# Kernel tuning notes

Measured on AMD Instinct MI355X. Metric: run time of the kernel, lower is better.

## Reference

```python
import jax, jax.numpy as jnp
import numpy as np

N_HEADS = 16

def setup_inputs() -> dict:
    key = jax.random.key(0)
    k1, k2 = jax.random.split(key)
    B, N, D = 2, 2048, 1024
    hidden_states = jax.random.normal(k1, (B, N, D), dtype=jnp.float32)
    # init std = initializer_range / sqrt(2 * num_layers * hidden_size)
    std = 0.02 / np.sqrt(2.0 * 24 * D)
    queries_weight = jax.random.normal(k2, (D, D), dtype=jnp.float32) * std
    return {"hidden_states": hidden_states, "queries_weight": queries_weight}

def reference(hidden_states, queries_weight):
    # DenseAttention, causal quadratic variant, multi-head, no relpe.
    B, N, D = hidden_states.shape
    H = N_HEADS
    hd = D // H
    # Q = X @ Wq, split into heads -> [B, H, N, hd]
    q = (hidden_states @ queries_weight).reshape(B, N, H, hd).transpose(0, 2, 1, 3)
    # K provided transposed per head -> [B, H, hd, N]; V -> [B, H, N, hd]
    xh = hidden_states.reshape(B, N, H, hd)
    k = xh.transpose(0, 2, 3, 1)
    v = xh.transpose(0, 2, 1, 3)
    # pre_attn = tril(Q @ K)  (no softmax in DenseAttention)
    pre_attn = jnp.tril(jnp.einsum('bhnd,bhdm->bhnm', q, k))  # [B,H,N,N]
    attn = jnp.einsum('bhnm,bhmd->bhnd', pre_attn, v)          # [B,H,N,hd]
    return attn.transpose(0, 2, 1, 3).reshape(B, N, D)
```

## Files before the change

kernel.cpp:

```cpp
#include <hip/hip_runtime.h>
#include <stdint.h>

#define Bz 2
#define Nseq 2048
#define Dm 1024
#define Hh 16
#define NCHUNK 32
#define BK 64

typedef _Float16 half_t;
typedef __attribute__((ext_vector_type(8))) _Float16 h8v;
typedef __attribute__((ext_vector_type(4))) _Float16 h4v;
typedef __attribute__((ext_vector_type(4))) float f4v;

#define GLDS(g, l)                                                        \
  __builtin_amdgcn_global_load_lds(                                       \
      (const __attribute__((address_space(1))) void*)(g),                 \
      (__attribute__((address_space(3))) void*)(l), 16, 0, 0)

__global__ __launch_bounds__(256) void prep_fused(const float* __restrict__ X,
                                                  const float* __restrict__ W,
                                                  half_t* __restrict__ Xf,
                                                  float* __restrict__ U,
                                                  half_t* __restrict__ WT) {
  __shared__ double smem_[2304];
  int bx = blockIdx.x;
  int t = threadIdx.x;
  if (bx < 1024) {
    half_t(*xt)[72] = (half_t(*)[72])smem_;
    half_t(*xtT)[72] = (half_t(*)[72])(smem_ + 1152);
    int c = bx & 31, h = (bx >> 5) & 15, b = bx >> 9;
    int r = t >> 2, c16 = (t & 3) * 16;
    {
      const float* src = X + ((size_t)b * Nseq + c * 64 + r) * Dm + h * 64 + c16;
      half_t* dXf = Xf + ((size_t)b * Nseq + c * 64 + r) * Dm + h * 64 + c16;
      h8v v0, v1;
#pragma unroll
      for (int j = 0; j < 8; j++) { v0[j] = (half_t)src[j]; v1[j] = (half_t)src[8 + j]; }
      *(h8v*)&xt[r][c16] = v0;
      *(h8v*)&xt[r][c16 + 8] = v1;
      *(h8v*)&dXf[0] = v0;
      *(h8v*)&dXf[8] = v1;
    }
    __syncthreads();
    {
      int d = r, mg = c16;
      h8v v0, v1;
#pragma unroll
      for (int j = 0; j < 8; j++) { v0[j] = xt[mg + j][d]; v1[j] = xt[mg + 8 + j][d]; }
      *(h8v*)&xtT[d][mg] = v0;
      *(h8v*)&xtT[d][mg + 8] = v1;
    }
    __syncthreads();
    int wave = t >> 6, lane = t & 63;
    int lrow = lane & 15, lk = (lane >> 4) * 8;
    h8v a0 = *(h8v*)&xtT[wave * 16 + lrow][lk];
    h8v a1 = *(h8v*)&xtT[wave * 16 + lrow][32 + lk];
    f4v acc[4] = {};
#pragma unroll
    for (int j = 0; j < 4; j++) {
      acc[j] = __builtin_amdgcn_mfma_f32_16x16x32_f16(a0, *(h8v*)&xtT[j * 16 + lrow][lk], acc[j], 0, 0, 0);
      acc[j] = __builtin_amdgcn_mfma_f32_16x16x32_f16(a1, *(h8v*)&xtT[j * 16 + lrow][32 + lk], acc[j], 0, 0, 0);
    }
    float* ub = U + (size_t)bx * 4096;
#pragma unroll
    for (int j = 0; j < 4; j++)
#pragma unroll
      for (int v = 0; v < 4; v++)
        ub[(size_t)(wave * 16 + (lane >> 4) * 4 + v) * 64 + j * 16 + (lane & 15)] = acc[j][v];
  } else {
    float(*tile)[65] = (float(*)[65])smem_;
    int bw = bx - 1024;
    int tk = bw >> 4, tn = bw & 15;
    int r = t >> 2, c0 = (t & 3) * 16;
    const float* src = W + (size_t)(tk * 64 + r) * Dm + tn * 64 + c0;
#pragma unroll
    for (int j = 0; j < 16; j++) tile[r][c0 + j] = src[j];
    __syncthreads();
    half_t* dst = WT + (size_t)(tn * 64 + r) * Dm + tk * 64 + c0;
    h8v v0, v1;
#pragma unroll
    for (int j = 0; j < 8; j++) {
      v0[j] = (half_t)(tile[c0 + j][r] * 4096.0f);
      v1[j] = (half_t)(tile[c0 + 8 + j][r] * 4096.0f);
    }
    *(h8v*)&dst[0] = v0;
    *(h8v*)&dst[8] = v1;
  }
}

__global__ __launch_bounds__(256) void qgemm16(const half_t* __restrict__ A,
                                               const half_t* __restrict__ Bw,
                                               half_t* __restrict__ Qs) {
  __shared__ half_t sA[128 * BK];
  __shared__ half_t sB[128 * BK];
  int bm = blockIdx.x >> 3, bn = blockIdx.x & 7;
  int t = threadIdx.x;
  int wave = t >> 6, lane = t & 63;
  int wr = wave >> 1, wc = wave & 1;
  int lrow = lane & 15, g4 = lane >> 4;

  int srow = wave * 32 + (lane >> 3);
  int scol = ((lane & 7) ^ (lane >> 3)) * 8;
  const half_t* pA = A + (size_t)(bm * 128 + srow) * Dm + scol;
  const half_t* pB = Bw + (size_t)(bn * 128 + srow) * Dm + scol;
  half_t* ldsA = sA + (size_t)(wave * 32) * BK;
  half_t* ldsB = sB + (size_t)(wave * 32) * BK;

  f4v acc[4][4] = {};
  for (int k0 = 0; k0 < Dm; k0 += BK) {
#pragma unroll
    for (int q = 0; q < 4; q++) {
      GLDS(pA + (size_t)q * 8 * Dm + k0, ldsA + q * 8 * BK);
      GLDS(pB + (size_t)q * 8 * Dm + k0, ldsB + q * 8 * BK);
    }
    __syncthreads();
#pragma unroll
    for (int ks = 0; ks < 2; ks++) {
      h8v af[4], bf[4];
#pragma unroll
      for (int i = 0; i < 4; i++) {
        int rowA = wr * 64 + i * 16 + lrow;
        uint offA = (uint)rowA * 128 + (((uint)(ks * 64 + g4 * 16)) ^ (uint)((rowA & 7) << 4));
        af[i] = *(const h8v*)((const char*)sA + offA);
        int rowB = wc * 64 + i * 16 + lrow;
        uint offB = (uint)rowB * 128 + (((uint)(ks * 64 + g4 * 16)) ^ (uint)((rowB & 7) << 4));
        bf[i] = *(const h8v*)((const char*)sB + offB);
      }
#pragma unroll
      for (int i = 0; i < 4; i++)
#pragma unroll
        for (int j = 0; j < 4; j++)
          acc[i][j] = __builtin_amdgcn_mfma_f32_16x16x32_f16(af[i], bf[j], acc[i][j], 0, 0, 0);
    }
    __syncthreads();
  }
#pragma unroll
  for (int i = 0; i < 4; i++)
#pragma unroll
    for (int j = 0; j < 4; j++) {
      int row = bm * 128 + wr * 64 + i * 16 + (lane >> 4) * 4;
      int col = bn * 128 + wc * 64 + j * 16 + (lane & 15);
#pragma unroll
      for (int v = 0; v < 4; v++)
        Qs[(size_t)(row + v) * Dm + col] = (half_t)(acc[i][j][v] * 0.0625f);
    }
}

__global__ __launch_bounds__(256) void prefix16(const float* __restrict__ U,
                                                half_t* __restrict__ S16) {
  int g = blockIdx.x * 256 + threadIdx.x;
  int bh = g >> 10, e4 = g & 1023;
  const float4* u = (const float4*)(U + (size_t)bh * NCHUNK * 4096) + e4;
  half_t* s = S16 + (size_t)bh * NCHUNK * 4096 + e4 * 4;
  float4 run = {0.f, 0.f, 0.f, 0.f};
  for (int c = 0; c < NCHUNK; c++) {
    h4v sv;
    sv[0] = (half_t)run.x; sv[1] = (half_t)run.y;
    sv[2] = (half_t)run.z; sv[3] = (half_t)run.w;
    *(h4v*)(s + (size_t)c * 4096) = sv;
    float4 uv = u[(size_t)c * 1024];
    run.x += uv.x; run.y += uv.y; run.z += uv.z; run.w += uv.w;
  }
}

__global__ __launch_bounds__(256) void attn16(const half_t* __restrict__ Xf,
                                              const half_t* __restrict__ Qs,
                                              const half_t* __restrict__ S16,
                                              float* __restrict__ out) {
  __shared__ half_t qs[64][72];
  __shared__ half_t ks[64][72];
  __shared__ half_t vts[64][72];
  __shared__ half_t ss[64][72];
  __shared__ half_t pt[64][72];
  int bx = blockIdx.x;
  int c = bx & 31, h = (bx >> 5) & 15, b = bx >> 9;
  int t = threadIdx.x;
  int r = t >> 2, c16 = (t & 3) * 16;
  {
    size_t rowoff = ((size_t)b * Nseq + c * 64 + r) * Dm + h * 64 + c16;
    *(h8v*)&qs[r][c16]     = *(const h8v*)(Qs + rowoff);
    *(h8v*)&qs[r][c16 + 8] = *(const h8v*)(Qs + rowoff + 8);
    *(h8v*)&ks[r][c16]     = *(const h8v*)(Xf + rowoff);
    *(h8v*)&ks[r][c16 + 8] = *(const h8v*)(Xf + rowoff + 8);
    size_t soff = ((size_t)(b * Hh + h) * NCHUNK + c) * 4096 + r * 64 + c16;
    *(h8v*)&ss[r][c16]     = *(const h8v*)(S16 + soff);
    *(h8v*)&ss[r][c16 + 8] = *(const h8v*)(S16 + soff + 8);
  }
  __syncthreads();
  int wave = t >> 6, lane = t & 63;
  int lrow = lane & 15, lk = (lane >> 4) * 8;
  h8v aq0 = *(h8v*)&qs[wave * 16 + lrow][lk];
  h8v aq1 = *(h8v*)&qs[wave * 16 + lrow][32 + lk];
  f4v p[4] = {};
#pragma unroll
  for (int j = 0; j < 4; j++) {
    p[j] = __builtin_amdgcn_mfma_f32_16x16x32_f16(aq0, *(h8v*)&ks[j * 16 + lrow][lk], p[j], 0, 0, 0);
    p[j] = __builtin_amdgcn_mfma_f32_16x16x32_f16(aq1, *(h8v*)&ks[j * 16 + lrow][32 + lk], p[j], 0, 0, 0);
  }
  {
    int d = r, mg = c16;
    h8v v0, v1;
#pragma unroll
    for (int j = 0; j < 8; j++) { v0[j] = ks[mg + j][d]; v1[j] = ks[mg + 8 + j][d]; }
    *(h8v*)&vts[d][mg] = v0;
    *(h8v*)&vts[d][mg + 8] = v1;
  }
  int orow = wave * 16 + (lane >> 4) * 4;
#pragma unroll
  for (int j = 0; j < 4; j++)
#pragma unroll
    for (int v = 0; v < 4; v++) {
      int rr = orow + v, mm = j * 16 + (lane & 15);
      pt[rr][mm] = (half_t)((mm <= rr) ? p[j][v] : 0.f);
    }
  __syncthreads();
  h8v ap0 = *(h8v*)&pt[wave * 16 + lrow][lk];
  h8v ap1 = *(h8v*)&pt[wave * 16 + lrow][32 + lk];
  f4v o[4] = {};
#pragma unroll
  for (int j = 0; j < 4; j++) {
    o[j] = __builtin_amdgcn_mfma_f32_16x16x32_f16(ap0, *(h8v*)&vts[j * 16 + lrow][lk], o[j], 0, 0, 0);
    o[j] = __builtin_amdgcn_mfma_f32_16x16x32_f16(ap1, *(h8v*)&vts[j * 16 + lrow][32 + lk], o[j], 0, 0, 0);
    o[j] = __builtin_amdgcn_mfma_f32_16x16x32_f16(aq0, *(h8v*)&ss[j * 16 + lrow][lk], o[j], 0, 0, 0);
    o[j] = __builtin_amdgcn_mfma_f32_16x16x32_f16(aq1, *(h8v*)&ss[j * 16 + lrow][32 + lk], o[j], 0, 0, 0);
  }
  float* dst = out + ((size_t)b * Nseq + c * 64) * Dm + h * 64;
#pragma unroll
  for (int j = 0; j < 4; j++)
#pragma unroll
    for (int v = 0; v < 4; v++)
      dst[(size_t)(orow + v) * Dm + j * 16 + (lane & 15)] = o[j][v] * 0.00390625f;
}

extern "C" void kernel_launch(void* const* d_in, const int* in_sizes, int n_in,
                              void* d_out, int out_size, void* d_ws, size_t ws_size,
                              hipStream_t stream) {
  const float* X = (const float*)d_in[0];
  const float* W = (const float*)d_in[1];
  float* out = (float*)d_out;

  float* U = (float*)d_ws;
  half_t* Xf = (half_t*)(U + 4194304);
  half_t* Qs = Xf + 4194304;
  half_t* S16 = Qs + 4194304;
  half_t* WT = S16 + 4194304;

  prep_fused<<<1280, 256, 0, stream>>>(X, W, Xf, U, WT);
  qgemm16<<<256, 256, 0, stream>>>(Xf, WT, Qs);
  prefix16<<<128, 256, 0, stream>>>(U, S16);
  attn16<<<1024, 256, 0, stream>>>(Xf, Qs, S16, out);
}
```

Measured before the change: 108.1 us.

## Fuse Q projection GEMM into attention kernel and store chunk sums in fp16

Merges the Q GEMM and the chunked attention into one kernel. Each block computes a 128x64 Q tile, which covers two sequence chunks of one head, using double-buffered LDS loads, then runs the causal intra-chunk attention on it directly from LDS. This removes the Qs global round trip and one launch. The per-chunk KᵀV partial sums are also stored in fp16 instead of fp32, halving that traffic at some precision risk. The trade-offs are a smaller GEMM tile (128x64 instead of 128x128) and a larger LDS footprint per block.

```diff
diff --git a/kernel.cpp b/kernel.cpp
--- a/kernel.cpp
+++ b/kernel.cpp
@@ -6,7 +6,7 @@
 #define Dm 1024
 #define Hh 16
 #define NCHUNK 32
-#define BK 64
+#define BKq 64
 
 typedef _Float16 half_t;
 typedef __attribute__((ext_vector_type(8))) _Float16 h8v;
@@ -21,7 +21,7 @@
 __global__ __launch_bounds__(256) void prep_fused(const float* __restrict__ X,
                                                   const float* __restrict__ W,
                                                   half_t* __restrict__ Xf,
-                                                  float* __restrict__ U,
+                                                  half_t* __restrict__ U16,
                                                   half_t* __restrict__ WT) {
   __shared__ double smem_[2304];
   int bx = blockIdx.x;
@@ -62,12 +62,12 @@
       acc[j] = __builtin_amdgcn_mfma_f32_16x16x32_f16(a0, *(h8v*)&xtT[j * 16 + lrow][lk], acc[j], 0, 0, 0);
       acc[j] = __builtin_amdgcn_mfma_f32_16x16x32_f16(a1, *(h8v*)&xtT[j * 16 + lrow][32 + lk], acc[j], 0, 0, 0);
     }
-    float* ub = U + (size_t)bx * 4096;
+    half_t* ub = U16 + (size_t)bx * 4096;
 #pragma unroll
     for (int j = 0; j < 4; j++)
 #pragma unroll
       for (int v = 0; v < 4; v++)
-        ub[(size_t)(wave * 16 + (lane >> 4) * 4 + v) * 64 + j * 16 + (lane & 15)] = acc[j][v];
+        ub[(size_t)(wave * 16 + (lane >> 4) * 4 + v) * 64 + j * 16 + (lane & 15)] = (half_t)acc[j][v];
   } else {
     float(*tile)[65] = (float(*)[65])smem_;
     int bw = bx - 1024;
@@ -89,148 +89,165 @@
   }
 }
 
-__global__ __launch_bounds__(256) void qgemm16(const half_t* __restrict__ A,
-                                               const half_t* __restrict__ Bw,
-                                               half_t* __restrict__ Qs) {
-  __shared__ half_t sA[128 * BK];
-  __shared__ half_t sB[128 * BK];
-  int bm = blockIdx.x >> 3, bn = blockIdx.x & 7;
+__global__ __launch_bounds__(256) void prefix16(const half_t* __restrict__ U16,
+                                                half_t* __restrict__ S16) {
+  int g = blockIdx.x * 256 + threadIdx.x;
+  int bh = g >> 10, e4 = g & 1023;
+  const half_t* u = U16 + (size_t)bh * NCHUNK * 4096 + e4 * 4;
+  half_t* s = S16 + (size_t)bh * NCHUNK * 4096 + e4 * 4;
+  float r0 = 0, r1 = 0, r2 = 0, r3 = 0;
+  for (int c = 0; c < NCHUNK; c++) {
+    h4v sv;
+    sv[0] = (half_t)r0; sv[1] = (half_t)r1; sv[2] = (half_t)r2; sv[3] = (half_t)r3;
+    *(h4v*)(s + (size_t)c * 4096) = sv;
+    h4v uv = *(const h4v*)(u + (size_t)c * 4096);
+    r0 += (float)uv[0]; r1 += (float)uv[1]; r2 += (float)uv[2]; r3 += (float)uv[3];
+  }
+}
+
+__global__ __launch_bounds__(256) void qgemm_attn(const half_t* __restrict__ Xf,
+                                                  const half_t* __restrict__ WT,
+                                                  const half_t* __restrict__ S16,
+                                                  float* __restrict__ out) {
+  __shared__ __attribute__((aligned(16))) char smem[55296];
+  int bid = blockIdx.x;
+  int logical = (bid & 7) * 64 + (bid >> 3);
+  int bm = logical >> 4;
+  int bn = logical & 15;
   int t = threadIdx.x;
   int wave = t >> 6, lane = t & 63;
   int wr = wave >> 1, wc = wave & 1;
   int lrow = lane & 15, g4 = lane >> 4;
 
-  int srow = wave * 32 + (lane >> 3);
+  int srowA = wave * 32 + (lane >> 3);
+  int srowB = wave * 16 + (lane >> 3);
   int scol = ((lane & 7) ^ (lane >> 3)) * 8;
-  const half_t* pA = A + (size_t)(bm * 128 + srow) * Dm + scol;
-  const half_t* pB = Bw + (size_t)(bn * 128 + srow) * Dm + scol;
-  half_t* ldsA = sA + (size_t)(wave * 32) * BK;
-  half_t* ldsB = sB + (size_t)(wave * 32) * BK;
-
-  f4v acc[4][4] = {};
-  for (int k0 = 0; k0 < Dm; k0 += BK) {
-#pragma unroll
-    for (int q = 0; q < 4; q++) {
-      GLDS(pA + (size_t)q * 8 * Dm + k0, ldsA + q * 8 * BK);
-      GLDS(pB + (size_t)q * 8 * Dm + k0, ldsB + q * 8 * BK);
-    }
-    __syncthreads();
-#pragma unroll
-    for (int ks = 0; ks < 2; ks++) {
-      h8v af[4], bf[4];
+  const half_t* pA = Xf + (size_t)(bm * 128 + srowA) * Dm + scol;
+  const half_t* pB = WT + (size_t)(bn * 64 + srowB) * Dm + scol;
+
+  f4v acc[4][2] = {};
+  {
+    half_t* dA = (half_t*)(smem) + (wave * 32) * BKq;
+    half_t* dB = (half_t*)(smem + 32768) + (wave * 16) * BKq;
+#pragma unroll
+    for (int q = 0; q < 4; q++) GLDS(pA + (size_t)q * 8 * Dm, dA + q * 8 * BKq);
+#pragma unroll
+    for (int q = 0; q < 2; q++) GLDS(pB + (size_t)q * 8 * Dm, dB + q * 8 * BKq);
+  }
+  __syncthreads();
+  for (int it = 0; it < 16; ++it) {
+    int cur = it & 1;
+    if (it < 15) {
+      int k1 = (it + 1) * BKq;
+      half_t* dA = (half_t*)(smem + (cur ^ 1) * 16384) + (wave * 32) * BKq;
+      half_t* dB = (half_t*)(smem + 32768 + (cur ^ 1) * 8192) + (wave * 16) * BKq;
+#pragma unroll
+      for (int q = 0; q < 4; q++) GLDS(pA + (size_t)q * 8 * Dm + k1, dA + q * 8 * BKq);
+#pragma unroll
+      for (int q = 0; q < 2; q++) GLDS(pB + (size_t)q * 8 * Dm + k1, dB + q * 8 * BKq);
+    }
+    const char* cA = smem + cur * 16384;
+    const char* cB = smem + 32768 + cur * 8192;
+#pragma unroll
+    for (int ks2 = 0; ks2 < 2; ks2++) {
+      h8v af[4], bf[2];
 #pragma unroll
       for (int i = 0; i < 4; i++) {
-        int rowA = wr * 64 + i * 16 + lrow;
-        uint offA = (uint)rowA * 128 + (((uint)(ks * 64 + g4 * 16)) ^ (uint)((rowA & 7) << 4));
-        af[i] = *(const h8v*)((const char*)sA + offA);
-        int rowB = wc * 64 + i * 16 + lrow;
-        uint offB = (uint)rowB * 128 + (((uint)(ks * 64 + g4 * 16)) ^ (uint)((rowB & 7) << 4));
-        bf[i] = *(const h8v*)((const char*)sB + offB);
+        int rA = wr * 64 + i * 16 + lrow;
+        uint offA = (uint)rA * 128 + (((uint)(ks2 * 64 + g4 * 16)) ^ (uint)((rA & 7) << 4));
+        af[i] = *(const h8v*)(cA + offA);
       }
 #pragma unroll
+      for (int j = 0; j < 2; j++) {
+        int rB = wc * 32 + j * 16 + lrow;
+        uint offB = (uint)rB * 128 + (((uint)(ks2 * 64 + g4 * 16)) ^ (uint)((rB & 7) << 4));
+        bf[j] = *(const h8v*)(cB + offB);
+      }
+#pragma unroll
       for (int i = 0; i < 4; i++)
 #pragma unroll
-        for (int j = 0; j < 4; j++)
+        for (int j = 0; j < 2; j++)
           acc[i][j] = __builtin_amdgcn_mfma_f32_16x16x32_f16(af[i], bf[j], acc[i][j], 0, 0, 0);
     }
     __syncthreads();
   }
-#pragma unroll
-  for (int i = 0; i < 4; i++)
+
+  half_t(*qs0)[72] = (half_t(*)[72])(smem);
+  half_t(*qs1)[72] = (half_t(*)[72])(smem + 9216);
+  half_t(*ks)[72]  = (half_t(*)[72])(smem + 18432);
+  half_t(*vts)[72] = (half_t(*)[72])(smem + 27648);
+  half_t(*ss)[72]  = (half_t(*)[72])(smem + 36864);
+  half_t(*pt)[72]  = (half_t(*)[72])(smem + 46080);
+  {
+    half_t(*qsw)[72] = wr ? qs1 : qs0;
+#pragma unroll
+    for (int i = 0; i < 4; i++)
+#pragma unroll
+      for (int j = 0; j < 2; j++)
+#pragma unroll
+        for (int v = 0; v < 4; v++)
+          qsw[i * 16 + (lane >> 4) * 4 + v][wc * 32 + j * 16 + (lane & 15)] =
+              (half_t)(acc[i][j][v] * 0.0625f);
+  }
+  int r = t >> 2, c16 = (t & 3) * 16;
+  int lk = g4 * 8;
+  int h = bn;
+  for (int cc = 0; cc < 2; ++cc) {
+    if (cc) __syncthreads();
+    int gc = bm * 2 + cc;
+    int b = gc >> 5, cl = gc & 31;
+    {
+      size_t rowoff = ((size_t)b * Nseq + cl * 64 + r) * Dm + h * 64 + c16;
+      *(h8v*)&ks[r][c16]     = *(const h8v*)(Xf + rowoff);
+      *(h8v*)&ks[r][c16 + 8] = *(const h8v*)(Xf + rowoff + 8);
+      size_t soff = ((size_t)(b * Hh + h) * NCHUNK + cl) * 4096 + r * 64 + c16;
+      *(h8v*)&ss[r][c16]     = *(const h8v*)(S16 + soff);
+      *(h8v*)&ss[r][c16 + 8] = *(const h8v*)(S16 + soff + 8);
+    }
+    __syncthreads();
+    half_t(*qsc)[72] = cc ? qs1 : qs0;
+    h8v aq0 = *(h8v*)&qsc[wave * 16 + lrow][lk];
+    h8v aq1 = *(h8v*)&qsc[wave * 16 + lrow][32 + lk];
+    f4v p[4] = {};
 #pragma unroll
     for (int j = 0; j < 4; j++) {
-      int row = bm * 128 + wr * 64 + i * 16 + (lane >> 4) * 4;
-      int col = bn * 128 + wc * 64 + j * 16 + (lane & 15);
+      p[j] = __builtin_amdgcn_mfma_f32_16x16x32_f16(aq0, *(h8v*)&ks[j * 16 + lrow][lk], p[j], 0, 0, 0);
+      p[j] = __builtin_amdgcn_mfma_f32_16x16x32_f16(aq1, *(h8v*)&ks[j * 16 + lrow][32 + lk], p[j], 0, 0, 0);
+    }
+    {
+      int d = r, mg = c16;
+      h8v v0, v1;
+#pragma unroll
+      for (int jj = 0; jj < 8; jj++) { v0[jj] = ks[mg + jj][d]; v1[jj] = ks[mg + 8 + jj][d]; }
+      *(h8v*)&vts[d][mg] = v0;
+      *(h8v*)&vts[d][mg + 8] = v1;
+    }
+    int orow = wave * 16 + (lane >> 4) * 4;
+#pragma unroll
+    for (int j = 0; j < 4; j++)
+#pragma unroll
+      for (int v = 0; v < 4; v++) {
+        int rr = orow + v, mm = j * 16 + (lane & 15);
+        pt[rr][mm] = (half_t)((mm <= rr) ? p[j][v] : 0.f);
+      }
+    __syncthreads();
+    h8v ap0 = *(h8v*)&pt[wave * 16 + lrow][lk];
+    h8v ap1 = *(h8v*)&pt[wave * 16 + lrow][32 + lk];
+    f4v o[4] = {};
+#pragma unroll
+    for (int j = 0; j < 4; j++) {
+      o[j] = __builtin_amdgcn_mfma_f32_16x16x32_f16(ap0, *(h8v*)&vts[j * 16 + lrow][lk], o[j], 0, 0, 0);
+      o[j] = __builtin_amdgcn_mfma_f32_16x16x32_f16(ap1, *(h8v*)&vts[j * 16 + lrow][32 + lk], o[j], 0, 0, 0);
+      o[j] = __builtin_amdgcn_mfma_f32_16x16x32_f16(aq0, *(h8v*)&ss[j * 16 + lrow][lk], o[j], 0, 0, 0);
+      o[j] = __builtin_amdgcn_mfma_f32_16x16x32_f16(aq1, *(h8v*)&ss[j * 16 + lrow][32 + lk], o[j], 0, 0, 0);
+    }
+    float* dst = out + ((size_t)b * Nseq + cl * 64) * Dm + h * 64;
+#pragma unroll
+    for (int j = 0; j < 4; j++)
 #pragma unroll
       for (int v = 0; v < 4; v++)
-        Qs[(size_t)(row + v) * Dm + col] = (half_t)(acc[i][j][v] * 0.0625f);
-    }
-}
-
-__global__ __launch_bounds__(256) void prefix16(const float* __restrict__ U,
-                                                half_t* __restrict__ S16) {
-  int g = blockIdx.x * 256 + threadIdx.x;
-  int bh = g >> 10, e4 = g & 1023;
-  const float4* u = (const float4*)(U + (size_t)bh * NCHUNK * 4096) + e4;
-  half_t* s = S16 + (size_t)bh * NCHUNK * 4096 + e4 * 4;
-  float4 run = {0.f, 0.f, 0.f, 0.f};
-  for (int c = 0; c < NCHUNK; c++) {
-    h4v sv;
-    sv[0] = (half_t)run.x; sv[1] = (half_t)run.y;
-    sv[2] = (half_t)run.z; sv[3] = (half_t)run.w;
-    *(h4v*)(s + (size_t)c * 4096) = sv;
-    float4 uv = u[(size_t)c * 1024];
-    run.x += uv.x; run.y += uv.y; run.z += uv.z; run.w += uv.w;
-  }
-}
-
-__global__ __launch_bounds__(256) void attn16(const half_t* __restrict__ Xf,
-                                              const half_t* __restrict__ Qs,
-                                              const half_t* __restrict__ S16,
-                                              float* __restrict__ out) {
-  __shared__ half_t qs[64][72];
-  __shared__ half_t ks[64][72];
-  __shared__ half_t vts[64][72];
-  __shared__ half_t ss[64][72];
-  __shared__ half_t pt[64][72];
-  int bx = blockIdx.x;
-  int c = bx & 31, h = (bx >> 5) & 15, b = bx >> 9;
-  int t = threadIdx.x;
-  int r = t >> 2, c16 = (t & 3) * 16;
-  {
-    size_t rowoff = ((size_t)b * Nseq + c * 64 + r) * Dm + h * 64 + c16;
-    *(h8v*)&qs[r][c16]     = *(const h8v*)(Qs + rowoff);
-    *(h8v*)&qs[r][c16 + 8] = *(const h8v*)(Qs + rowoff + 8);
-    *(h8v*)&ks[r][c16]     = *(const h8v*)(Xf + rowoff);
-    *(h8v*)&ks[r][c16 + 8] = *(const h8v*)(Xf + rowoff + 8);
-    size_t soff = ((size_t)(b * Hh + h) * NCHUNK + c) * 4096 + r * 64 + c16;
-    *(h8v*)&ss[r][c16]     = *(const h8v*)(S16 + soff);
-    *(h8v*)&ss[r][c16 + 8] = *(const h8v*)(S16 + soff + 8);
-  }
-  __syncthreads();
-  int wave = t >> 6, lane = t & 63;
-  int lrow = lane & 15, lk = (lane >> 4) * 8;
-  h8v aq0 = *(h8v*)&qs[wave * 16 + lrow][lk];
-  h8v aq1 = *(h8v*)&qs[wave * 16 + lrow][32 + lk];
-  f4v p[4] = {};
-#pragma unroll
-  for (int j = 0; j < 4; j++) {
-    p[j] = __builtin_amdgcn_mfma_f32_16x16x32_f16(aq0, *(h8v*)&ks[j * 16 + lrow][lk], p[j], 0, 0, 0);
-    p[j] = __builtin_amdgcn_mfma_f32_16x16x32_f16(aq1, *(h8v*)&ks[j * 16 + lrow][32 + lk], p[j], 0, 0, 0);
-  }
-  {
-    int d = r, mg = c16;
-    h8v v0, v1;
-#pragma unroll
-    for (int j = 0; j < 8; j++) { v0[j] = ks[mg + j][d]; v1[j] = ks[mg + 8 + j][d]; }
-    *(h8v*)&vts[d][mg] = v0;
-    *(h8v*)&vts[d][mg + 8] = v1;
-  }
-  int orow = wave * 16 + (lane >> 4) * 4;
-#pragma unroll
-  for (int j = 0; j < 4; j++)
-#pragma unroll
-    for (int v = 0; v < 4; v++) {
-      int rr = orow + v, mm = j * 16 + (lane & 15);
-      pt[rr][mm] = (half_t)((mm <= rr) ? p[j][v] : 0.f);
-    }
-  __syncthreads();
-  h8v ap0 = *(h8v*)&pt[wave * 16 + lrow][lk];
-  h8v ap1 = *(h8v*)&pt[wave * 16 + lrow][32 + lk];
-  f4v o[4] = {};
-#pragma unroll
-  for (int j = 0; j < 4; j++) {
-    o[j] = __builtin_amdgcn_mfma_f32_16x16x32_f16(ap0, *(h8v*)&vts[j * 16 + lrow][lk], o[j], 0, 0, 0);
-    o[j] = __builtin_amdgcn_mfma_f32_16x16x32_f16(ap1, *(h8v*)&vts[j * 16 + lrow][32 + lk], o[j], 0, 0, 0);
-    o[j] = __builtin_amdgcn_mfma_f32_16x16x32_f16(aq0, *(h8v*)&ss[j * 16 + lrow][lk], o[j], 0, 0, 0);
-    o[j] = __builtin_amdgcn_mfma_f32_16x16x32_f16(aq1, *(h8v*)&ss[j * 16 + lrow][32 + lk], o[j], 0, 0, 0);
-  }
-  float* dst = out + ((size_t)b * Nseq + c * 64) * Dm + h * 64;
-#pragma unroll
-  for (int j = 0; j < 4; j++)
-#pragma unroll
-    for (int v = 0; v < 4; v++)
-      dst[(size_t)(orow + v) * Dm + j * 16 + (lane & 15)] = o[j][v] * 0.00390625f;
+        dst[(size_t)(orow + v) * Dm + j * 16 + (lane & 15)] = o[j][v] * 0.00390625f;
+  }
 }
 
 extern "C" void kernel_launch(void* const* d_in, const int* in_sizes, int n_in,
@@ -240,14 +257,12 @@
   const float* W = (const float*)d_in[1];
   float* out = (float*)d_out;
 
-  float* U = (float*)d_ws;
-  half_t* Xf = (half_t*)(U + 4194304);
-  half_t* Qs = Xf + 4194304;
-  half_t* S16 = Qs + 4194304;
+  half_t* U16 = (half_t*)d_ws;
+  half_t* Xf = U16 + 4194304;
+  half_t* S16 = Xf + 4194304;
   half_t* WT = S16 + 4194304;
 
-  prep_fused<<<1280, 256, 0, stream>>>(X, W, Xf, U, WT);
-  qgemm16<<<256, 256, 0, stream>>>(Xf, WT, Qs);
-  prefix16<<<128, 256, 0, stream>>>(U, S16);
-  attn16<<<1024, 256, 0, stream>>>(Xf, Qs, S16, out);
-}
+  prep_fused<<<1280, 256, 0, stream>>>(X, W, Xf, U16, WT);
+  prefix16<<<128, 256, 0, stream>>>(U16, S16);
+  qgemm_attn<<<512, 256, 0, stream>>>(Xf, WT, S16, out);
+}
```

Result: faster. 96.49 us (-10.7%).
